# Optimization experiments

Measured on AMD Instinct MI355X. Metric: run time of the kernel, lower is better.

Reference implementation:

```python
import jax, jax.numpy as jnp
import numpy as np

N_GRAPH = 1024
NODES_PER_GRAPH = 512
TOTAL_NODES = N_GRAPH * NODES_PER_GRAPH  # 524288
D_FEAT = 128
EPS = 1e-06


def setup_inputs() -> dict:
    key = jax.random.key(0)
    k1, k2, k3, k4 = jax.random.split(key, 4)
    x = jax.random.normal(k1, (TOTAL_NODES, D_FEAT), dtype=jnp.float32)
    # per-graph node counts; sum(n_node) == TOTAL_NODES (equal-size graphs)
    n_node = jnp.full((N_GRAPH,), NODES_PER_GRAPH, dtype=jnp.int32)
    mean_scale = jax.random.uniform(k2, (D_FEAT,), dtype=jnp.float32)
    scale = jax.random.uniform(k3, (D_FEAT,), dtype=jnp.float32)
    bias = jax.random.normal(k4, (D_FEAT,), dtype=jnp.float32)
    return {"x": x, "n_node": n_node, "mean_scale": mean_scale, "scale": scale, "bias": bias}


def reference(x, n_node, mean_scale, scale, bias):
    n_graph = n_node.shape[0]
    total_nodes = x.shape[0]
    node_graph_idx = jnp.repeat(jnp.arange(n_graph), n_node, axis=0,
                                total_repeat_length=total_nodes)  # [N]
    ones = jnp.ones((total_nodes, 1), dtype=x.dtype)
    counts = jax.ops.segment_sum(ones, node_graph_idx, n_graph)  # [G,1]
    # per-graph mean, broadcast back to nodes
    mean_g = jax.ops.segment_sum(x, node_graph_idx, n_graph) / counts  # [G,D]
    mean_n = jnp.repeat(mean_g, n_node, axis=0, total_repeat_length=total_nodes)
    # NOTE: faithful to source - the mean is scaled by mean_scale BEFORE both
    # the centering and the variance computation.
    mean_n = mean_n * mean_scale
    y = x - mean_n
    var_g = jax.ops.segment_sum((x - mean_n) ** 2, node_graph_idx, n_graph) / counts
    var_n = jnp.repeat(var_g, n_node, axis=0, total_repeat_length=total_nodes)
    mul = jax.lax.rsqrt(var_n + EPS) * scale
    y = y * mul + bias
    return y.astype(x.dtype)
```

## Files before the change

kernel.cpp:

```cpp
#include <hip/hip_runtime.h>

#define D_FEAT 128
#define F4 (D_FEAT / 4)
#define BLOCK 1024
#define FAST_NODES 512
#define PER_THREAD (FAST_NODES * F4 / BLOCK)
#define EPS 1e-6f

__global__ __launch_bounds__(BLOCK, 4) void graphnorm_kernel(
    const float* __restrict__ x,
    const int* __restrict__ n_node,
    const float* __restrict__ mean_scale,
    const float* __restrict__ scale,
    const float* __restrict__ bias,
    float* __restrict__ y,
    int n_graph)
{
    const int g    = blockIdx.x;
    const int t    = threadIdx.x;
    const int lane = t & 63;
    const int wave = t >> 6;
    const int grp  = t & 31;
    const int nsub = t >> 5;

    __shared__ int    s_int[16];
    __shared__ float4 s_sum[16][32];
    __shared__ float4 s_sq [16][32];
    __shared__ float4 s_a[32];
    __shared__ float4 s_b[32];
    __shared__ int    s_off;

    int my = 0;
    for (int i = t; i < g; i += BLOCK) my += n_node[i];
    #pragma unroll
    for (int o = 32; o; o >>= 1) my += __shfl_down(my, o);
    if (lane == 0) s_int[wave] = my;
    __syncthreads();
    if (t == 0) {
        int tot = 0;
        #pragma unroll
        for (int w = 0; w < 16; w++) tot += s_int[w];
        s_off = tot;
    }
    __syncthreads();
    const int   node0 = s_off;
    const int   cnt   = n_node[g];
    const float inv   = 1.0f / (float)cnt;

    const float4* __restrict__ xg = (const float4*)x + (size_t)node0 * F4;
    float4*       __restrict__ yg = (float4*)y       + (size_t)node0 * F4;

    float4 sum = make_float4(0.f, 0.f, 0.f, 0.f);
    float4 sq  = make_float4(0.f, 0.f, 0.f, 0.f);

    float4 v[PER_THREAD];
    const bool fast = (cnt == FAST_NODES);

    if (fast) {
        #pragma unroll
        for (int i = 0; i < PER_THREAD; i++) {
            const int node = nsub + 32 * i;
            v[i] = xg[(size_t)node * F4 + grp];
            sum.x += v[i].x; sum.y += v[i].y; sum.z += v[i].z; sum.w += v[i].w;
            sq.x  += v[i].x * v[i].x; sq.y += v[i].y * v[i].y;
            sq.z  += v[i].z * v[i].z; sq.w += v[i].w * v[i].w;
        }
    } else {
        for (int node = nsub; node < cnt; node += 32) {
            float4 val = xg[(size_t)node * F4 + grp];
            sum.x += val.x; sum.y += val.y; sum.z += val.z; sum.w += val.w;
            sq.x  += val.x * val.x; sq.y += val.y * val.y;
            sq.z  += val.z * val.z; sq.w += val.w * val.w;
        }
    }

    sum.x += __shfl_down(sum.x, 32); sum.y += __shfl_down(sum.y, 32);
    sum.z += __shfl_down(sum.z, 32); sum.w += __shfl_down(sum.w, 32);
    sq.x  += __shfl_down(sq.x, 32);  sq.y  += __shfl_down(sq.y, 32);
    sq.z  += __shfl_down(sq.z, 32);  sq.w  += __shfl_down(sq.w, 32);
    if (lane < 32) { s_sum[wave][lane] = sum; s_sq[wave][lane] = sq; }
    __syncthreads();

    if (t < 32) {
        float4 S = make_float4(0.f, 0.f, 0.f, 0.f);
        float4 Q = make_float4(0.f, 0.f, 0.f, 0.f);
        #pragma unroll
        for (int w = 0; w < 16; w++) {
            float4 a4 = s_sum[w][t];
            float4 b4 = s_sq[w][t];
            S.x += a4.x; S.y += a4.y; S.z += a4.z; S.w += a4.w;
            Q.x += b4.x; Q.y += b4.y; Q.z += b4.z; Q.w += b4.w;
        }
        const float4 ms = ((const float4*)mean_scale)[t];
        const float4 sc = ((const float4*)scale)[t];
        const float4 bs = ((const float4*)bias)[t];

        float4 A, B;
        {
            float mean = S.x * inv, m = mean * ms.x;
            float var  = Q.x * inv - 2.f * m * mean + m * m;
            A.x = rsqrtf(var + EPS) * sc.x; B.x = bs.x - m * A.x;
        }
        {
            float mean = S.y * inv, m = mean * ms.y;
            float var  = Q.y * inv - 2.f * m * mean + m * m;
            A.y = rsqrtf(var + EPS) * sc.y; B.y = bs.y - m * A.y;
        }
        {
            float mean = S.z * inv, m = mean * ms.z;
            float var  = Q.z * inv - 2.f * m * mean + m * m;
            A.z = rsqrtf(var + EPS) * sc.z; B.z = bs.z - m * A.z;
        }
        {
            float mean = S.w * inv, m = mean * ms.w;
            float var  = Q.w * inv - 2.f * m * mean + m * m;
            A.w = rsqrtf(var + EPS) * sc.w; B.w = bs.w - m * A.w;
        }
        s_a[t] = A; s_b[t] = B;
    }
    __syncthreads();

    const float4 a = s_a[grp];
    const float4 b = s_b[grp];

    if (fast) {
        #pragma unroll
        for (int i = 0; i < PER_THREAD; i++) {
            const int node = nsub + 32 * i;
            float4 r;
            r.x = v[i].x * a.x + b.x;
            r.y = v[i].y * a.y + b.y;
            r.z = v[i].z * a.z + b.z;
            r.w = v[i].w * a.w + b.w;
            yg[(size_t)node * F4 + grp] = r;
        }
    } else {
        for (int node = nsub; node < cnt; node += 32) {
            float4 val = xg[(size_t)node * F4 + grp];
            float4 r;
            r.x = val.x * a.x + b.x;
            r.y = val.y * a.y + b.y;
            r.z = val.z * a.z + b.z;
            r.w = val.w * a.w + b.w;
            yg[(size_t)node * F4 + grp] = r;
        }
    }
}

extern "C" void kernel_launch(void* const* d_in, const int* in_sizes, int n_in,
                              void* d_out, int out_size, void* d_ws, size_t ws_size,
                              hipStream_t stream) {
    const float* x          = (const float*)d_in[0];
    const int*   n_node     = (const int*)d_in[1];
    const float* mean_scale = (const float*)d_in[2];
    const float* scale      = (const float*)d_in[3];
    const float* bias       = (const float*)d_in[4];
    float*       y          = (float*)d_out;

    const int n_graph = in_sizes[1];

    graphnorm_kernel<<<n_graph, BLOCK, 0, stream>>>(
        x, n_node, mean_scale, scale, bias, y, n_graph);
}
```

Baseline: 451.0 us.

## Drop register-cached tile, re-read x in second pass with nontemporal stores

```diff
diff --git a/kernel.cpp b/kernel.cpp
--- a/kernel.cpp
+++ b/kernel.cpp
@@ -2,12 +2,13 @@
 
 #define D_FEAT 128
 #define F4 (D_FEAT / 4)
-#define BLOCK 1024
-#define FAST_NODES 512
-#define PER_THREAD (FAST_NODES * F4 / BLOCK)
+#define BLOCK 512
+#define NSUB (BLOCK / F4)
 #define EPS 1e-6f
 
-__global__ __launch_bounds__(BLOCK, 4) void graphnorm_kernel(
+typedef float nat4 __attribute__((ext_vector_type(4)));
+
+__global__ __launch_bounds__(BLOCK, 8) void graphnorm_kernel(
     const float* __restrict__ x,
     const int* __restrict__ n_node,
     const float* __restrict__ mean_scale,
@@ -23,9 +24,9 @@
     const int grp  = t & 31;
     const int nsub = t >> 5;
 
-    __shared__ int    s_int[16];
-    __shared__ float4 s_sum[16][32];
-    __shared__ float4 s_sq [16][32];
+    __shared__ int    s_int[8];
+    __shared__ float4 s_sum[8][32];
+    __shared__ float4 s_sq [8][32];
     __shared__ float4 s_a[32];
     __shared__ float4 s_b[32];
     __shared__ int    s_off;
@@ -39,7 +40,7 @@
     if (t == 0) {
         int tot = 0;
         #pragma unroll
-        for (int w = 0; w < 16; w++) tot += s_int[w];
+        for (int w = 0; w < 8; w++) tot += s_int[w];
         s_off = tot;
     }
     __syncthreads();
@@ -53,25 +54,12 @@
     float4 sum = make_float4(0.f, 0.f, 0.f, 0.f);
     float4 sq  = make_float4(0.f, 0.f, 0.f, 0.f);
 
-    float4 v[PER_THREAD];
-    const bool fast = (cnt == FAST_NODES);
-
-    if (fast) {
-        #pragma unroll
-        for (int i = 0; i < PER_THREAD; i++) {
-            const int node = nsub + 32 * i;
-            v[i] = xg[(size_t)node * F4 + grp];
-            sum.x += v[i].x; sum.y += v[i].y; sum.z += v[i].z; sum.w += v[i].w;
-            sq.x  += v[i].x * v[i].x; sq.y += v[i].y * v[i].y;
-            sq.z  += v[i].z * v[i].z; sq.w += v[i].w * v[i].w;
-        }
-    } else {
-        for (int node = nsub; node < cnt; node += 32) {
-            float4 val = xg[(size_t)node * F4 + grp];
-            sum.x += val.x; sum.y += val.y; sum.z += val.z; sum.w += val.w;
-            sq.x  += val.x * val.x; sq.y += val.y * val.y;
-            sq.z  += val.z * val.z; sq.w += val.w * val.w;
-        }
+    #pragma unroll 4
+    for (int node = nsub; node < cnt; node += NSUB) {
+        float4 val = xg[(size_t)node * F4 + grp];
+        sum.x += val.x; sum.y += val.y; sum.z += val.z; sum.w += val.w;
+        sq.x  += val.x * val.x; sq.y += val.y * val.y;
+        sq.z  += val.z * val.z; sq.w += val.w * val.w;
     }
 
     sum.x += __shfl_down(sum.x, 32); sum.y += __shfl_down(sum.y, 32);
@@ -85,7 +73,7 @@
         float4 S = make_float4(0.f, 0.f, 0.f, 0.f);
         float4 Q = make_float4(0.f, 0.f, 0.f, 0.f);
         #pragma unroll
-        for (int w = 0; w < 16; w++) {
+        for (int w = 0; w < 8; w++) {
             float4 a4 = s_sum[w][t];
             float4 b4 = s_sq[w][t];
             S.x += a4.x; S.y += a4.y; S.z += a4.z; S.w += a4.w;
@@ -123,27 +111,15 @@
     const float4 a = s_a[grp];
     const float4 b = s_b[grp];
 
-    if (fast) {
-        #pragma unroll
-        for (int i = 0; i < PER_THREAD; i++) {
-            const int node = nsub + 32 * i;
-            float4 r;
-            r.x = v[i].x * a.x + b.x;
-            r.y = v[i].y * a.y + b.y;
-            r.z = v[i].z * a.z + b.z;
-            r.w = v[i].w * a.w + b.w;
-            yg[(size_t)node * F4 + grp] = r;
-        }
-    } else {
-        for (int node = nsub; node < cnt; node += 32) {
-            float4 val = xg[(size_t)node * F4 + grp];
-            float4 r;
-            r.x = val.x * a.x + b.x;
-            r.y = val.y * a.y + b.y;
-            r.z = val.z * a.z + b.z;
-            r.w = val.w * a.w + b.w;
-            yg[(size_t)node * F4 + grp] = r;
-        }
+    #pragma unroll 4
+    for (int node = nsub; node < cnt; node += NSUB) {
+        float4 val = xg[(size_t)node * F4 + grp];
+        nat4 r;
+        r.x = val.x * a.x + b.x;
+        r.y = val.y * a.y + b.y;
+        r.z = val.z * a.z + b.z;
+        r.w = val.w * a.w + b.w;
+        __builtin_nontemporal_store(r, (nat4*)&yg[(size_t)node * F4 + grp]);
     }
 }
 
```

Result: slower. 464.7 us (+3.0%).
